# Optimization experiments

Hardware: AMD Instinct MI355X
Metric: run time of the kernel (lower is better)

## Reference

```python
import jax, jax.numpy as jnp
import numpy as np

DIM = 1024
H = 16
DH = DIM // H
NF = 64
EPS = 1e-6


def setup_inputs() -> dict:
    key = jax.random.key(0)
    ks = jax.random.split(key, 10)
    B, L = 4, 4096
    s = 1.0 / np.sqrt(DIM)
    x = jax.random.normal(ks[0], (B, L, DIM), dtype=jnp.float32)
    Wq = jax.random.normal(ks[1], (DIM, DIM), dtype=jnp.float32) * s
    Wk = jax.random.normal(ks[2], (DIM, DIM), dtype=jnp.float32) * s
    Wv = jax.random.normal(ks[3], (DIM, DIM), dtype=jnp.float32) * s
    Wo = jax.random.normal(ks[4], (DIM, DIM), dtype=jnp.float32) * s
    bq = jax.random.normal(ks[5], (DIM,), dtype=jnp.float32) * s
    bk = jax.random.normal(ks[6], (DIM,), dtype=jnp.float32) * s
    bv = jax.random.normal(ks[7], (DIM,), dtype=jnp.float32) * s
    bo = jax.random.normal(ks[8], (DIM,), dtype=jnp.float32) * s
    # random-feature buffer: [num_repeats=1, H, DH, NF]; use repeat 0
    Wrf = jax.random.normal(ks[9], (1, H, DH, NF), dtype=jnp.float32)
    return {"x": x, "Wq": Wq, "bq": bq, "Wk": Wk, "bk": bk, "Wv": Wv,
            "bv": bv, "Wo": Wo, "bo": bo, "Wrf": Wrf}


def reference(x, Wq, bq, Wk, bk, Wv, bv, Wo, bo, Wrf):
    B, L, _ = x.shape
    W0 = Wrf[0]  # [H, DH, NF]

    def split_heads(y):
        return y.reshape(B, L, H, DH).transpose(0, 2, 1, 3)  # [B,H,L,DH]

    q = split_heads(x @ Wq.T + bq)
    k = split_heads(x @ Wk.T + bk)
    v = split_heads(x @ Wv.T + bv)

    # key summary: logits [B,H,L,NF], softmax over flattened (L*NF)
    logits = jnp.einsum('bhld,hdf->bhlf', k, W0) \
             - 0.5 * jnp.sum(k * k, axis=-1, keepdims=True)
    alpha = jax.nn.softmax(logits.reshape(B, H, L * NF), axis=2)
    alpha = alpha.reshape(B, H, L, NF)
    N = jnp.einsum('bhlf,bhld->bhfd', alpha, v)  # [B,H,NF,DH]
    D = jnp.sum(alpha, axis=2)                   # [B,H,NF]

    # query feature map: per-position softmax over features
    phi = jax.nn.softmax(jnp.einsum('bhld,hdf->bhlf', q, W0), axis=-1)

    num = jnp.einsum('bhlf,bhfd->bhld', phi, N)
    den = jnp.einsum('bhlf,bhf->bhl', phi, D)
    out = num / (den[..., None] + EPS)

    ctx = out.transpose(0, 2, 1, 3).reshape(B, L, DIM)
    return ctx @ Wo.T + bo
```

## Files before the change

### kernel.cpp

```cpp
#include <hip/hip_runtime.h>
#include <hip/hip_bf16.h>

constexpr int NB   = 4;
constexpr int SL   = 4096;
constexpr int DIMC = 1024;
constexpr int NH   = 16;
constexpr int DHC  = 64;
constexpr int NFC  = 64;
constexpr int NCHK = 8;
constexpr float FEPS = 1e-6f;

typedef __attribute__((ext_vector_type(8))) short bf16x8_t;
typedef __attribute__((ext_vector_type(4))) float f32x4_t;
typedef __attribute__((ext_vector_type(4))) short s16x4_t;

__device__ __forceinline__ void load_lds_16B(const short* g, short* l) {
  __builtin_amdgcn_global_load_lds(
      (__attribute__((address_space(1))) void*)(g),
      (__attribute__((address_space(3))) void*)(l), 16, 0, 0);
}

__global__ __launch_bounds__(256) void cast_f32_to_bf16(
    const float* __restrict__ in, short* __restrict__ out, int n)
{
  const int i = (blockIdx.x * 256 + threadIdx.x) * 4;
  if (i >= n) return;
  const f32x4_t v = *(const f32x4_t*)(in + i);
  s16x4_t o;
#pragma unroll
  for (int j = 0; j < 4; j++) {
    __hip_bfloat16 h = __float2bfloat16(v[j]);
    o[j] = *(short*)&h;
  }
  *(s16x4_t*)(out + i) = o;
}

__global__ __launch_bounds__(256) void cast3_kernel(
    const float* __restrict__ a, const float* __restrict__ b,
    const float* __restrict__ c, short* __restrict__ oa,
    short* __restrict__ ob, short* __restrict__ oc)
{
  const float* in  = blockIdx.y == 0 ? a : (blockIdx.y == 1 ? b : c);
  short*       out = blockIdx.y == 0 ? oa : (blockIdx.y == 1 ? ob : oc);
  const int i = (blockIdx.x * 256 + threadIdx.x) * 4;
  const f32x4_t v = *(const f32x4_t*)(in + i);
  s16x4_t o;
#pragma unroll
  for (int j = 0; j < 4; j++) {
    __hip_bfloat16 h = __float2bfloat16(v[j]);
    o[j] = *(short*)&h;
  }
  *(s16x4_t*)(out + i) = o;
}

__global__ __launch_bounds__(256) void prep_w0t_kernel(
    const float* __restrict__ Wrf, short* __restrict__ Whi, short* __restrict__ Wlo)
{
  const int h = blockIdx.x;
  for (int t = threadIdx.x; t < 4096; t += 256) {
    const int f = t >> 6, dh = t & 63;
    const float w = Wrf[(size_t)h * 4096 + dh * 64 + f];
    __hip_bfloat16 hi = __float2bfloat16(w);
    const float rem = w - __bfloat162float(hi);
    __hip_bfloat16 lo = __float2bfloat16(rem);
    Whi[(size_t)h * 4096 + t] = *(short*)&hi;
    Wlo[(size_t)h * 4096 + t] = *(short*)&lo;
  }
}

__global__ __launch_bounds__(256) void fuse_w0_kernel(
    const float* __restrict__ Wq, const float* __restrict__ bq,
    const float* __restrict__ Wrf,
    short* __restrict__ Wfh, short* __restrict__ Wfl, float* __restrict__ bqf)
{
  const int h = blockIdx.x, cb = blockIdx.y;
  __shared__ float sWq[64][64];
  __shared__ float sW0[64][64];
  for (int idx = threadIdx.x; idx < 4096; idx += 256) {
    const int d = idx >> 6, e = idx & 63;
    sWq[d][e] = Wq[(size_t)(h * 64 + d) * 1024 + cb * 64 + e];
    sW0[d][e] = Wrf[(size_t)h * 4096 + d * 64 + e];
  }
  __syncthreads();
  for (int idx = threadIdx.x; idx < 4096; idx += 256) {
    const int f = idx >> 6, cc = idx & 63;
    float acc = 0.f;
#pragma unroll
    for (int d = 0; d < 64; d++) acc = fmaf(sWq[d][cc], sW0[d][f], acc);
    const __hip_bfloat16 hi = __float2bfloat16(acc);
    const float rem = acc - __bfloat162float(hi);
    const __hip_bfloat16 lo = __float2bfloat16(rem);
    Wfh[(size_t)(h * 64 + f) * 1024 + cb * 64 + cc] = *(const short*)&hi;
    Wfl[(size_t)(h * 64 + f) * 1024 + cb * 64 + cc] = *(const short*)&lo;
  }
  if (cb == 0 && threadIdx.x < 64) {
    const int f = threadIdx.x;
    float acc = 0.f;
#pragma unroll
    for (int d = 0; d < 64; d++) acc = fmaf(bq[h * 64 + d], sW0[d][f], acc);
    bqf[h * 64 + f] = acc;
  }
}

__global__ __launch_bounds__(256) void gemm_out_kernel(
    const short* __restrict__ A, const short* __restrict__ W,
    const float* __restrict__ bias, float* __restrict__ C0)
{
  constexpr int K = 1024, N = 1024;
  const int lane = threadIdx.x & 63;
  const int wid  = threadIdx.x >> 6;
  const int sub  = lane & 15;
  const int quad = lane >> 4;
  const int wr   = (wid >> 1) * 64;
  const int wc   = (wid & 1) * 64;
  const int row0 = blockIdx.x * 128;
  const int col0 = blockIdx.y * 128;

  __shared__ short As[128 * 64];
  __shared__ short Bs[128 * 64];

  f32x4_t acc[4][4] = {};

  const int srow = lane >> 3;
  for (int k0 = 0; k0 < K; k0 += 64) {
#pragma unroll
    for (int t = 0; t < 4; t++) {
      const int R   = wid * 32 + t * 8;
      const int row = R + srow;
      const int c   = (lane & 7) ^ (row & 7);
      load_lds_16B(A + (size_t)(row0 + row) * K + k0 + c * 8, As + R * 64);
      load_lds_16B(W + (size_t)(col0 + row) * K + k0 + c * 8, Bs + R * 64);
    }
    __syncthreads();

    bf16x8_t a[2][4], b[2][4];
#pragma unroll
    for (int ks = 0; ks < 2; ks++) {
#pragma unroll
      for (int i = 0; i < 4; i++) {
        const int ra = wr + i * 16 + sub;
        a[ks][i] = *(const bf16x8_t*)(As + ra * 64 + (((ks * 4 + quad) ^ (ra & 7)) * 8));
        const int rb = wc + i * 16 + sub;
        b[ks][i] = *(const bf16x8_t*)(Bs + rb * 64 + (((ks * 4 + quad) ^ (rb & 7)) * 8));
      }
    }
#pragma unroll
    for (int ks = 0; ks < 2; ks++)
#pragma unroll
      for (int i = 0; i < 4; i++)
#pragma unroll
        for (int j = 0; j < 4; j++)
          acc[i][j] = __builtin_amdgcn_mfma_f32_16x16x32_bf16(a[ks][i], b[ks][j], acc[i][j], 0, 0, 0);
    __syncthreads();
  }

  const int rb0 = row0 + wr;
  const int cb0 = col0 + wc;
#pragma unroll
  for (int j = 0; j < 4; j++) {
    const int col = cb0 + j * 16 + sub;
    const float bv = bias[col];
#pragma unroll
    for (int i = 0; i < 4; i++) {
      const int row = rb0 + i * 16 + quad * 4;
#pragma unroll
      for (int r = 0; r < 4; r++)
        C0[(size_t)(row + r) * N + col] = acc[i][j][r] + bv;
    }
  }
}

__global__ __launch_bounds__(256) void gemm_kv_kernel(
    const short* __restrict__ A, const short* __restrict__ Wk,
    const short* __restrict__ Wv, const float* __restrict__ bk,
    const float* __restrict__ bv,
    __hip_bfloat16* __restrict__ chi, __hip_bfloat16* __restrict__ clo,
    float* __restrict__ Ks, __hip_bfloat16* __restrict__ vT)
{
  constexpr int K = 1024, N = 1024;
  const int lane = threadIdx.x & 63;
  const int wid  = threadIdx.x >> 6;
  const int sub  = lane & 15;
  const int quad = lane >> 4;
  const int wr   = (wid >> 1) * 64;
  const int wc   = (wid & 1) * 64;
  const int row0 = blockIdx.x * 128;
  const int col0 = blockIdx.y * 128;

  __shared__ short As[128 * 64];
  __shared__ short Bks[128 * 64];
  __shared__ short Bvs[128 * 64];

  f32x4_t accK[4][4] = {};
  f32x4_t accV[4][4] = {};

  const int srow = lane >> 3;
  for (int k0 = 0; k0 < K; k0 += 64) {
#pragma unroll
    for (int t = 0; t < 4; t++) {
      const int R   = wid * 32 + t * 8;
      const int row = R + srow;
      const int c   = (lane & 7) ^ (row & 7);
      load_lds_16B(A  + (size_t)(row0 + row) * K + k0 + c * 8, As  + R * 64);
      load_lds_16B(Wk + (size_t)(col0 + row) * K + k0 + c * 8, Bks + R * 64);
      load_lds_16B(Wv + (size_t)(col0 + row) * K + k0 + c * 8, Bvs + R * 64);
    }
    __syncthreads();

#pragma unroll
    for (int ks = 0; ks < 2; ks++) {
      bf16x8_t a[4], bb[4];
#pragma unroll
      for (int i = 0; i < 4; i++) {
        const int ra = wr + i * 16 + sub;
        a[i] = *(const bf16x8_t*)(As + ra * 64 + (((ks * 4 + quad) ^ (ra & 7)) * 8));
      }
#pragma unroll
      for (int j = 0; j < 4; j++) {
        const int rb = wc + j * 16 + sub;
        bb[j] = *(const bf16x8_t*)(Bks + rb * 64 + (((ks * 4 + quad) ^ (rb & 7)) * 8));
      }
#pragma unroll
      for (int i = 0; i < 4; i++)
#pragma unroll
        for (int j = 0; j < 4; j++)
          accK[i][j] = __builtin_amdgcn_mfma_f32_16x16x32_bf16(a[i], bb[j], accK[i][j], 0, 0, 0);
#pragma unroll
      for (int j = 0; j < 4; j++) {
        const int rb = wc + j * 16 + sub;
        bb[j] = *(const bf16x8_t*)(Bvs + rb * 64 + (((ks * 4 + quad) ^ (rb & 7)) * 8));
      }
#pragma unroll
      for (int i = 0; i < 4; i++)
#pragma unroll
        for (int j = 0; j < 4; j++)
          accV[i][j] = __builtin_amdgcn_mfma_f32_16x16x32_bf16(bb[j], a[i], accV[i][j], 0, 0, 0);
    }
    __syncthreads();
  }

  const int rb0 = row0 + wr;
  const int cb0 = col0 + wc;

  {
    float s[4][4];
#pragma unroll
    for (int i = 0; i < 4; i++)
#pragma unroll
      for (int r = 0; r < 4; r++) s[i][r] = 0.f;
#pragma unroll
    for (int j = 0; j < 4; j++) {
      const int col = cb0 + j * 16 + sub;
      const float bvv = bk[col];
#pragma unroll
      for (int i = 0; i < 4; i++) {
        const int row = rb0 + i * 16 + quad * 4;
#pragma unroll
        for (int r = 0; r < 4; r++) {
          const float val = accK[i][j][r] + bvv;
          const __hip_bfloat16 hi = __float2bfloat16(val);
          const float rem = val - __bfloat162float(hi);
          chi[(size_t)(row + r) * N + col] = hi;
          clo[(size_t)(row + r) * N + col] = __float2bfloat16(rem);
          s[i][r] = fmaf(val, val, s[i][r]);
        }
      }
    }
    const int head = cb0 >> 6;
#pragma unroll
    for (int o = 1; o < 16; o <<= 1)
#pragma unroll
      for (int i = 0; i < 4; i++)
#pragma unroll
        for (int r = 0; r < 4; r++) s[i][r] += __shfl_xor(s[i][r], o);
    if (sub == 0) {
#pragma unroll
      for (int i = 0; i < 4; i++)
#pragma unroll
        for (int r = 0; r < 4; r++)
          Ks[(size_t)(rb0 + i * 16 + quad * 4 + r) * NH + head] = s[i][r];
    }
  }

  {
    const int bb    = row0 >> 12;
    const int lbase = rb0 - (bb << 12);
#pragma unroll
    for (int j = 0; j < 4; j++) {
#pragma unroll
      for (int r = 0; r < 4; r++) {
        const int col = cb0 + j * 16 + quad * 4 + r;
        const int h = col >> 6, d = col & 63;
        const float bvv = bv[col];
        const size_t rowbase = ((size_t)((bb * NH + h) * 64 + d)) * (size_t)SL;
#pragma unroll
        for (int i = 0; i < 4; i++) {
          const int l = lbase + i * 16 + sub;
          const int pos = (l & ~127) | (((((l >> 3) & 15) ^ (d & 15)) << 3) | (l & 7));
          vT[rowbase + pos] = __float2bfloat16(accV[i][j][r] + bvv);
        }
      }
    }
  }
}

__global__ __launch_bounds__(256) void gemm_phi_kernel(
    const short* __restrict__ A, const short* __restrict__ Wh,
    const short* __restrict__ Wl, const float* __restrict__ bqf,
    const float* __restrict__ Df, short* __restrict__ ehi,
    short* __restrict__ elo, float* __restrict__ sbuf)
{
  constexpr int K = 1024;
  const int lane = threadIdx.x & 63;
  const int wid  = threadIdx.x >> 6;
  const int sub  = lane & 15;
  const int quad = lane >> 4;
  const int wr   = (wid >> 1) * 64;
  const int wc   = (wid & 1) * 64;
  const int row0 = blockIdx.x * 128;
  const int col0 = blockIdx.y * 128;

  __shared__ short As[128 * 64];
  __shared__ short Bhs[128 * 64];
  __shared__ short Bls[128 * 64];

  f32x4_t acc[4][4] = {};

  const int srow = lane >> 3;
  for (int k0 = 0; k0 < K; k0 += 64) {
#pragma unroll
    for (int t = 0; t < 4; t++) {
      const int R   = wid * 32 + t * 8;
      const int row = R + srow;
      const int c   = (lane & 7) ^ (row & 7);
      load_lds_16B(A  + (size_t)(row0 + row) * K + k0 + c * 8, As  + R * 64);
      load_lds_16B(Wh + (size_t)(col0 + row) * K + k0 + c * 8, Bhs + R * 64);
      load_lds_16B(Wl + (size_t)(col0 + row) * K + k0 + c * 8, Bls + R * 64);
    }
    __syncthreads();

#pragma unroll
    for (int ks = 0; ks < 2; ks++) {
      bf16x8_t a[4], bh[4], bl[4];
#pragma unroll
      for (int i = 0; i < 4; i++) {
        const int ra = wr + i * 16 + sub;
        a[i] = *(const bf16x8_t*)(As + ra * 64 + (((ks * 4 + quad) ^ (ra & 7)) * 8));
        const int rb = wc + i * 16 + sub;
        bh[i] = *(const bf16x8_t*)(Bhs + rb * 64 + (((ks * 4 + quad) ^ (rb & 7)) * 8));
        bl[i] = *(const bf16x8_t*)(Bls + rb * 64 + (((ks * 4 + quad) ^ (rb & 7)) * 8));
      }
#pragma unroll
      for (int i = 0; i < 4; i++)
#pragma unroll
        for (int j = 0; j < 4; j++) {
          acc[i][j] = __builtin_amdgcn_mfma_f32_16x16x32_bf16(a[i], bh[j], acc[i][j], 0, 0, 0);
          acc[i][j] = __builtin_amdgcn_mfma_f32_16x16x32_bf16(a[i], bl[j], acc[i][j], 0, 0, 0);
        }
      __syncthreads();
    }
  }

  const int rb0 = row0 + wr;
  const int cb0 = col0 + wc;
  const int b   = row0 >> 12;
  const int h   = cb0 >> 6;
  float bv[4], Dl[4];
#pragma unroll
  for (int j = 0; j < 4; j++) {
    const int f = j * 16 + sub;
    bv[j] = bqf[h * 64 + f];
    Dl[j] = Df[(b * NH + h) * 64 + f];
  }
#pragma unroll
  for (int i = 0; i < 4; i++) {
#pragma unroll
    for (int r = 0; r < 4; r++) {
      float v[4];
#pragma unroll
      for (int j = 0; j < 4; j++) v[j] = acc[i][j][r] + bv[j];
      float mx = fmaxf(fmaxf(v[0], v[1]), fmaxf(v[2], v[3]));
#pragma unroll
      for (int o = 1; o < 16; o <<= 1) mx = fmaxf(mx, __shfl_xor(mx, o));
      float e[4], se = 0.f, dt = 0.f;
#pragma unroll
      for (int j = 0; j < 4; j++) {
        e[j] = __expf(v[j] - mx);
        se += e[j];
        dt = fmaf(e[j], Dl[j], dt);
      }
#pragma unroll
      for (int o = 1; o < 16; o <<= 1) { se += __shfl_xor(se, o); dt += __shfl_xor(dt, o); }

      const int row = rb0 + i * 16 + quad * 4 + r;
      const size_t base = (size_t)row * DIMC + h * 64;
#pragma unroll
      for (int j = 0; j < 4; j++) {
        const __hip_bfloat16 hi = __float2bfloat16(e[j]);
        const float rem = e[j] - __bfloat162float(hi);
        const __hip_bfloat16 lo = __float2bfloat16(rem);
        ehi[base + j * 16 + sub] = *(const short*)&hi;
        elo[base + j * 16 + sub] = *(const short*)&lo;
      }
      if (sub == 0) sbuf[row * NH + h] = 1.f / (dt + FEPS * se);
    }
  }
}

__global__ __launch_bounds__(256) void kv_fused_kernel(
    const short* __restrict__ khi, const short* __restrict__ klo,
    const short* __restrict__ W0h, const short* __restrict__ W0l,
    const float* __restrict__ ksq, const short* __restrict__ vT,
    float* __restrict__ pN, float* __restrict__ pD)
{
  const int chunk = blockIdx.x, h = blockIdx.y, b = blockIdx.z;
  const int tid  = threadIdx.x;
  const int lane = tid & 63, wid = tid >> 6;
  const int sub  = lane & 15, quad = lane >> 4;

  __shared__ short vTs[64 * 128];
  __shared__ short w0hs[64 * 64];
  __shared__ short w0ls[64 * 64];
  __shared__ short uh[128 * 64];
  __shared__ short ul[128 * 64];

  f32x4_t accN[4] = {};
  f32x4_t accD = {};
  bf16x8_t bones;
#pragma unroll
  for (int e = 0; e < 8; e++) bones[e] = (sub == 0) ? (short)0x3F80 : (short)0;

#pragma unroll
  for (int t = 0; t < 2; t++) {
    const int R   = wid * 16 + t * 8;
    const int row = R + (lane >> 3);
    const int c   = (lane & 7) ^ (row & 7);
    load_lds_16B(W0h + (size_t)h * 4096 + row * 64 + c * 8, w0hs + R * 64);
    load_lds_16B(W0l + (size_t)h * 4096 + row * 64 + c * 8, w0ls + R * 64);
  }

  const size_t vbase = ((size_t)((b * NH + h) * 64)) * (size_t)SL;
  const int fbase = (wid * 16 + sub) * 128;

  for (int it = 0; it < 4; ++it) {
    const int l0 = chunk * 512 + it * 128;

#pragma unroll
    for (int q = 0; q < 4; q++) {
      const int dbase = wid * 16 + q * 4;
      const int d = dbase + (lane >> 4);
      load_lds_16B(vT + vbase + (size_t)d * SL + l0 + (lane & 15) * 8,
                   vTs + dbase * 128);
    }
#pragma unroll
    for (int t = 0; t < 4; t++) {
      const int R   = wid * 32 + t * 8;
      const int row = R + (lane >> 3);
      const int c   = (lane & 7) ^ (row & 7);
      const size_t src = (size_t)(b * SL + l0 + row) * DIMC + h * 64 + c * 8;
      load_lds_16B(khi + src, uh + R * 64);
      load_lds_16B(klo + src, ul + R * 64);
    }
    __syncthreads();

    f32x4_t kacc[2][4] = {};
#pragma unroll
    for (int ks = 0; ks < 2; ks++) {
      bf16x8_t ah[2], al[2], b0[4], b1[4];
#pragma unroll
      for (int i = 0; i < 2; i++) {
        const int ra  = wid * 32 + i * 16 + sub;
        const int off = ra * 64 + (((ks * 4 + quad) ^ (ra & 7)) * 8);
        ah[i] = *(const bf16x8_t*)(uh + off);
        al[i] = *(const bf16x8_t*)(ul + off);
      }
#pragma unroll
      for (int j = 0; j < 4; j++) {
        const int rb  = j * 16 + sub;
        const int off = rb * 64 + (((ks * 4 + quad) ^ (rb & 7)) * 8);
        b0[j] = *(const bf16x8_t*)(w0hs + off);
        b1[j] = *(const bf16x8_t*)(w0ls + off);
      }
#pragma unroll
      for (int i = 0; i < 2; i++)
#pragma unroll
        for (int j = 0; j < 4; j++) {
          kacc[i][j] = __builtin_amdgcn_mfma_f32_16x16x32_bf16(ah[i], b0[j], kacc[i][j], 0, 0, 0);
          kacc[i][j] = __builtin_amdgcn_mfma_f32_16x16x32_bf16(al[i], b0[j], kacc[i][j], 0, 0, 0);
          kacc[i][j] = __builtin_amdgcn_mfma_f32_16x16x32_bf16(ah[i], b1[j], kacc[i][j], 0, 0, 0);
        }
    }
    __syncthreads();

#pragma unroll
    for (int i = 0; i < 2; i++) {
#pragma unroll
      for (int r = 0; r < 4; r++) {
        const int tok = wid * 32 + i * 16 + quad * 4 + r;
        const float kq = 0.5f * ksq[(size_t)(b * SL + l0 + tok) * NH + h];
#pragma unroll
        for (int j = 0; j < 4; j++) {
          const int f = j * 16 + sub;
          const float wv = __expf(kacc[i][j][r] - kq);
          const __hip_bfloat16 hi = __float2bfloat16(wv);
          const float rem = wv - __bfloat162float(hi);
          const __hip_bfloat16 lo = __float2bfloat16(rem);
          const int p = f * 128 + (((((tok >> 3) & 15) ^ (f & 15)) << 3) | (tok & 7));
          uh[p] = *(const short*)&hi;
          ul[p] = *(const short*)&lo;
        }
      }
    }
    __syncthreads();

#pragma unroll
    for (int ks = 0; ks < 4; ks++) {
      const int ch = ks * 4 + quad;
      const bf16x8_t ah = *(const bf16x8_t*)(uh + fbase + ((ch ^ sub) << 3));
      const bf16x8_t al = *(const bf16x8_t*)(ul + fbase + ((ch ^ sub) << 3));
      accD = __builtin_amdgcn_mfma_f32_16x16x32_bf16(ah, bones, accD, 0, 0, 0);
      accD = __builtin_amdgcn_mfma_f32_16x16x32_bf16(al, bones, accD, 0, 0, 0);
#pragma unroll
      for (int j = 0; j < 4; j++) {
        const bf16x8_t bv = *(const bf16x8_t*)(vTs + (j * 16 + sub) * 128 + ((ch ^ sub) << 3));
        accN[j] = __builtin_amdgcn_mfma_f32_16x16x32_bf16(ah, bv, accN[j], 0, 0, 0);
        accN[j] = __builtin_amdgcn_mfma_f32_16x16x32_bf16(al, bv, accN[j], 0, 0, 0);
      }
    }
    __syncthreads();
  }

  const size_t pbase = (size_t)((b * NH + h) * NCHK + chunk);
#pragma unroll
  for (int j = 0; j < 4; j++)
#pragma unroll
    for (int r = 0; r < 4; r++)
      pN[pbase * 4096 + (wid * 16 + quad * 4 + r) * 64 + j * 16 + sub] = accN[j][r];
  if (sub == 0) {
#pragma unroll
    for (int r = 0; r < 4; r++)
      pD[pbase * 64 + wid * 16 + quad * 4 + r] = accD[r];
  }
}

__global__ __launch_bounds__(256) void combine_nd_kernel(
    const float* __restrict__ pN, const float* __restrict__ pD,
    short* __restrict__ NfTh, short* __restrict__ NfTl, float* __restrict__ Df)
{
  const int bh = blockIdx.x, seg = blockIdx.y;
  __shared__ float sInv;
  float dsum = 0.f;
  if (threadIdx.x < 64) {
    for (int c = 0; c < NCHK; c++)
      dsum += pD[(size_t)(bh * NCHK + c) * 64 + threadIdx.x];
    float s = dsum;
#pragma unroll
    for (int o = 32; o; o >>= 1) s += __shfl_xor(s, o);
    if (threadIdx.x == 0) sInv = 1.f / s;
  }
  __syncthreads();
  const float inv = sInv;
  if (seg == 0 && threadIdx.x < 64) Df[bh * 64 + threadIdx.x] = dsum * inv;
  const int t = seg * 256 + threadIdx.x;
  float acc = 0.f;
  for (int c = 0; c < NCHK; c++)
    acc += pN[((size_t)(bh * NCHK + c)) * 4096 + t];
  const float val = acc * inv;
  const int f = t >> 6, d = t & 63;
  const __hip_bfloat16 hi = __float2bfloat16(val);
  const float rem = val - __bfloat162float(hi);
  const __hip_bfloat16 lo = __float2bfloat16(rem);
  NfTh[(size_t)bh * 4096 + d * 64 + f] = *(const short*)&hi;
  NfTl[(size_t)bh * 4096 + d * 64 + f] = *(const short*)&lo;
}

__global__ __launch_bounds__(256) void ctx_gemm_kernel(
    const short* __restrict__ ehi, const short* __restrict__ elo,
    const short* __restrict__ NfTh, const short* __restrict__ NfTl,
    const float* __restrict__ sbuf, __hip_bfloat16* __restrict__ ctx)
{
  const int lane = threadIdx.x & 63, wid = threadIdx.x >> 6;
  const int sub = lane & 15, quad = lane >> 4;
  const int h = blockIdx.y;
  const int tok0 = blockIdx.x * 128 + wid * 32;
  const int b = blockIdx.x >> 5;
  const short* Bh = NfTh + ((size_t)(b * NH + h)) * 4096;
  const short* Bl = NfTl + ((size_t)(b * NH + h)) * 4096;

  f32x4_t acc[2][4] = {};
#pragma unroll
  for (int ks = 0; ks < 2; ks++) {
    const int ko = ks * 32 + quad * 8;
    bf16x8_t ah[2], al[2], bh[4], bl[4];
#pragma unroll
    for (int i = 0; i < 2; i++) {
      const size_t base = (size_t)(tok0 + i * 16 + sub) * DIMC + h * 64 + ko;
      ah[i] = *(const bf16x8_t*)(ehi + base);
      al[i] = *(const bf16x8_t*)(elo + base);
    }
#pragma unroll
    for (int j = 0; j < 4; j++) {
      const size_t base = (size_t)(j * 16 + sub) * 64 + ko;
      bh[j] = *(const bf16x8_t*)(Bh + base);
      bl[j] = *(const bf16x8_t*)(Bl + base);
    }
#pragma unroll
    for (int i = 0; i < 2; i++)
#pragma unroll
      for (int j = 0; j < 4; j++) {
        acc[i][j] = __builtin_amdgcn_mfma_f32_16x16x32_bf16(ah[i], bh[j], acc[i][j], 0, 0, 0);
        acc[i][j] = __builtin_amdgcn_mfma_f32_16x16x32_bf16(al[i], bh[j], acc[i][j], 0, 0, 0);
        acc[i][j] = __builtin_amdgcn_mfma_f32_16x16x32_bf16(ah[i], bl[j], acc[i][j], 0, 0, 0);
      }
  }
#pragma unroll
  for (int i = 0; i < 2; i++)
#pragma unroll
    for (int r = 0; r < 4; r++) {
      const int token = tok0 + i * 16 + quad * 4 + r;
      const float sv = sbuf[token * NH + h];
#pragma unroll
      for (int j = 0; j < 4; j++)
        ctx[(size_t)token * DIMC + h * 64 + j * 16 + sub] =
            __float2bfloat16(acc[i][j][r] * sv);
    }
}

extern "C" void kernel_launch(void* const* d_in, const int* in_sizes, int n_in,
                              void* d_out, int out_size, void* d_ws, size_t ws_size,
                              hipStream_t stream) {
  (void)in_sizes; (void)n_in; (void)out_size; (void)ws_size;
  const float* x   = (const float*)d_in[0];
  const float* Wq  = (const float*)d_in[1];
  const float* bq  = (const float*)d_in[2];
  const float* Wk  = (const float*)d_in[3];
  const float* bk  = (const float*)d_in[4];
  const float* Wv  = (const float*)d_in[5];
  const float* bv  = (const float*)d_in[6];
  const float* Wo  = (const float*)d_in[7];
  const float* bo  = (const float*)d_in[8];
  const float* Wrf = (const float*)d_in[9];
  float* out = (float*)d_out;

  constexpr size_t MiB = 1u << 20;
  constexpr size_t KiB = 1u << 10;
  constexpr size_t NTOK = (size_t)NB * SL;
  constexpr size_t XN   = NTOK * DIMC;
  constexpr size_t WN   = (size_t)DIMC * DIMC;

  char* ws = (char*)d_ws;
  short* xb   = (short*)(ws);
  short* Wkb  = (short*)(ws + 32 * MiB);
  short* Wvb  = (short*)(ws + 34 * MiB);
  short* Wob  = (short*)(ws + 36 * MiB);
  short* W0Th = (short*)(ws + 40 * MiB);
  short* W0Tl = (short*)(ws + 40 * MiB + 128 * KiB);
  float* bqf  = (float*)(ws + 40 * MiB + 256 * KiB);
  float* ksq  = (float*)(ws + 41 * MiB);
  float* sbuf = (float*)(ws + 42 * MiB);
  float* pD   = (float*)(ws + 43 * MiB);
  short* NfTh = (short*)(ws + 43 * MiB + 512 * KiB);
  short* NfTl = (short*)(ws + 44 * MiB);
  float* Df   = (float*)(ws + 44 * MiB + 512 * KiB);
  float* pN   = (float*)(ws + 45 * MiB);
  __hip_bfloat16* khi = (__hip_bfloat16*)(ws + 109 * MiB);
  __hip_bfloat16* klo = (__hip_bfloat16*)(ws + 141 * MiB);
  short* vTb  = (short*)(ws + 173 * MiB);
  short* Wqfh = (short*)(ws + 173 * MiB);
  short* Wqfl = (short*)(ws + 175 * MiB);
  short* ehi  = (short*)(ws + 45 * MiB);
  short* elo  = (short*)(ws + 77 * MiB);
  __hip_bfloat16* ctxb = (__hip_bfloat16*)xb;

  const dim3 blk(256);

  cast_f32_to_bf16<<<dim3(XN / 1024), blk, 0, stream>>>(x, xb, (int)XN);
  cast3_kernel<<<dim3(WN / 1024, 3), blk, 0, stream>>>(Wk, Wv, Wo, Wkb, Wvb, Wob);
  prep_w0t_kernel<<<dim3(NH), blk, 0, stream>>>(Wrf, W0Th, W0Tl);

  const dim3 gg(NTOK / 128, DIMC / 128);
  gemm_kv_kernel<<<gg, blk, 0, stream>>>(xb, Wkb, Wvb, bk, bv,
                                         khi, klo, ksq, (__hip_bfloat16*)vTb);

  kv_fused_kernel<<<dim3(NCHK, NH, NB), blk, 0, stream>>>(
      (const short*)khi, (const short*)klo, W0Th, W0Tl, ksq, vTb, pN, pD);
  fuse_w0_kernel<<<dim3(NH, 16), blk, 0, stream>>>(Wq, bq, Wrf, Wqfh, Wqfl, bqf);
  combine_nd_kernel<<<dim3(NB * NH, 16), blk, 0, stream>>>(pN, pD, NfTh, NfTl, Df);

  gemm_phi_kernel<<<gg, blk, 0, stream>>>(xb, Wqfh, Wqfl, bqf, Df, ehi, elo, sbuf);
  ctx_gemm_kernel<<<dim3(NTOK / 128, NH), blk, 0, stream>>>(
      ehi, elo, NfTh, NfTl, sbuf, ctxb);

  gemm_out_kernel<<<gg, blk, 0, stream>>>((const short*)ctxb, Wob, bo, out);
}
```

Measured before the change: 468.7 us.

## Split fused K/V GEMM into templated launches; stream phi B tiles from global

Splits the fused K/V projection GEMM into two launches of a templated single-weight GEMM, one per epilogue mode. The combined kernel kept two accumulator sets and three LDS tiles, which limited occupancy. The phi GEMM also stops staging the hi/lo Wqf tiles in LDS and loads them straight from global memory into registers, with one barrier per k-step instead of one per sub-step. In exchange, the x tile is read twice across the two GEMMs, there is an extra launch, and the global B loads in the phi GEMM may hurt latency hiding.

```diff
diff --git a/kernel.cpp b/kernel.cpp
--- a/kernel.cpp
+++ b/kernel.cpp
@@ -102,9 +102,11 @@
   }
 }
 
-__global__ __launch_bounds__(256) void gemm_out_kernel(
+template <int MODE>
+__global__ __launch_bounds__(256) void gemm_lds_kernel(
     const short* __restrict__ A, const short* __restrict__ W,
-    const float* __restrict__ bias, float* __restrict__ C0)
+    const float* __restrict__ bias, void* __restrict__ C0,
+    void* __restrict__ C1, float* __restrict__ Ks)
 {
   constexpr int K = 1024, N = 1024;
   const int lane = threadIdx.x & 63;
@@ -149,33 +151,85 @@
 #pragma unroll
       for (int i = 0; i < 4; i++)
 #pragma unroll
-        for (int j = 0; j < 4; j++)
-          acc[i][j] = __builtin_amdgcn_mfma_f32_16x16x32_bf16(a[ks][i], b[ks][j], acc[i][j], 0, 0, 0);
+        for (int j = 0; j < 4; j++) {
+          if constexpr (MODE == 5)
+            acc[i][j] = __builtin_amdgcn_mfma_f32_16x16x32_bf16(b[ks][j], a[ks][i], acc[i][j], 0, 0, 0);
+          else
+            acc[i][j] = __builtin_amdgcn_mfma_f32_16x16x32_bf16(a[ks][i], b[ks][j], acc[i][j], 0, 0, 0);
+        }
     __syncthreads();
   }
 
   const int rb0 = row0 + wr;
   const int cb0 = col0 + wc;
-#pragma unroll
-  for (int j = 0; j < 4; j++) {
-    const int col = cb0 + j * 16 + sub;
-    const float bv = bias[col];
-#pragma unroll
-    for (int i = 0; i < 4; i++) {
-      const int row = rb0 + i * 16 + quad * 4;
-#pragma unroll
-      for (int r = 0; r < 4; r++)
-        C0[(size_t)(row + r) * N + col] = acc[i][j][r] + bv;
-    }
-  }
-}
-
-__global__ __launch_bounds__(256) void gemm_kv_kernel(
-    const short* __restrict__ A, const short* __restrict__ Wk,
-    const short* __restrict__ Wv, const float* __restrict__ bk,
-    const float* __restrict__ bv,
-    __hip_bfloat16* __restrict__ chi, __hip_bfloat16* __restrict__ clo,
-    float* __restrict__ Ks, __hip_bfloat16* __restrict__ vT)
+  if constexpr (MODE == 3) {
+    __hip_bfloat16* chi = (__hip_bfloat16*)C0;
+    __hip_bfloat16* clo = (__hip_bfloat16*)C1;
+    float s[4][4];
+#pragma unroll
+    for (int i = 0; i < 4; i++)
+#pragma unroll
+      for (int r = 0; r < 4; r++) s[i][r] = 0.f;
+#pragma unroll
+    for (int j = 0; j < 4; j++) {
+      const int col = cb0 + j * 16 + sub;
+      const float bv = bias[col];
+#pragma unroll
+      for (int i = 0; i < 4; i++) {
+        const int row = rb0 + i * 16 + quad * 4;
+#pragma unroll
+        for (int r = 0; r < 4; r++) {
+          const float val = acc[i][j][r] + bv;
+          const __hip_bfloat16 hi = __float2bfloat16(val);
+          const float rem = val - __bfloat162float(hi);
+          chi[(size_t)(row + r) * N + col] = hi;
+          clo[(size_t)(row + r) * N + col] = __float2bfloat16(rem);
+          s[i][r] = fmaf(val, val, s[i][r]);
+        }
+      }
+    }
+    {
+      const int head = cb0 >> 6;
+#pragma unroll
+      for (int o = 1; o < 16; o <<= 1)
+#pragma unroll
+        for (int i = 0; i < 4; i++)
+#pragma unroll
+          for (int r = 0; r < 4; r++) s[i][r] += __shfl_xor(s[i][r], o);
+      if (sub == 0) {
+#pragma unroll
+        for (int i = 0; i < 4; i++)
+#pragma unroll
+          for (int r = 0; r < 4; r++)
+            Ks[(size_t)(rb0 + i * 16 + quad * 4 + r) * NH + head] = s[i][r];
+      }
+    }
+  } else if constexpr (MODE == 5) {
+    __hip_bfloat16* vT = (__hip_bfloat16*)C0;
+    const int bb    = row0 >> 12;
+    const int lbase = rb0 - (bb << 12);
+#pragma unroll
+    for (int j = 0; j < 4; j++) {
+#pragma unroll
+      for (int r = 0; r < 4; r++) {
+        const int col = cb0 + j * 16 + quad * 4 + r;
+        const int h = col >> 6, d = col & 63;
+        const float bv = bias[col];
+        const size_t rowbase = ((size_t)((bb * NH + h) * 64 + d)) * (size_t)SL;
+#pragma unroll
+        for (int i = 0; i < 4; i++) {
+          const int l = lbase + i * 16 + sub;
+          const int pos = (l & ~127) | (((((l >> 3) & 15) ^ (d & 15)) << 3) | (l & 7));
+          vT[rowbase + pos] = __float2bfloat16(acc[i][j][r] + bv);
+        }
+      }
+    }
+  }
+}
+
+__global__ __launch_bounds__(256) void gemm_out_kernel(
+    const short* __restrict__ A, const short* __restrict__ W,
+    const float* __restrict__ bias, float* __restrict__ C0)
 {
   constexpr int K = 1024, N = 1024;
   const int lane = threadIdx.x & 63;
@@ -188,11 +242,9 @@
   const int col0 = blockIdx.y * 128;
 
   __shared__ short As[128 * 64];
-  __shared__ short Bks[128 * 64];
-  __shared__ short Bvs[128 * 64];
-
-  f32x4_t accK[4][4] = {};
-  f32x4_t accV[4][4] = {};
+  __shared__ short Bs[128 * 64];
+
+  f32x4_t acc[4][4] = {};
 
   const int srow = lane >> 3;
   for (int k0 = 0; k0 < K; k0 += 64) {
@@ -201,105 +253,44 @@
       const int R   = wid * 32 + t * 8;
       const int row = R + srow;
       const int c   = (lane & 7) ^ (row & 7);
-      load_lds_16B(A  + (size_t)(row0 + row) * K + k0 + c * 8, As  + R * 64);
-      load_lds_16B(Wk + (size_t)(col0 + row) * K + k0 + c * 8, Bks + R * 64);
-      load_lds_16B(Wv + (size_t)(col0 + row) * K + k0 + c * 8, Bvs + R * 64);
-    }
-    __syncthreads();
-
+      load_lds_16B(A + (size_t)(row0 + row) * K + k0 + c * 8, As + R * 64);
+      load_lds_16B(W + (size_t)(col0 + row) * K + k0 + c * 8, Bs + R * 64);
+    }
+    __syncthreads();
+
+    bf16x8_t a[2][4], b[2][4];
 #pragma unroll
     for (int ks = 0; ks < 2; ks++) {
-      bf16x8_t a[4], bb[4];
 #pragma unroll
       for (int i = 0; i < 4; i++) {
         const int ra = wr + i * 16 + sub;
-        a[i] = *(const bf16x8_t*)(As + ra * 64 + (((ks * 4 + quad) ^ (ra & 7)) * 8));
-      }
-#pragma unroll
-      for (int j = 0; j < 4; j++) {
-        const int rb = wc + j * 16 + sub;
-        bb[j] = *(const bf16x8_t*)(Bks + rb * 64 + (((ks * 4 + quad) ^ (rb & 7)) * 8));
-      }
+        a[ks][i] = *(const bf16x8_t*)(As + ra * 64 + (((ks * 4 + quad) ^ (ra & 7)) * 8));
+        const int rb = wc + i * 16 + sub;
+        b[ks][i] = *(const bf16x8_t*)(Bs + rb * 64 + (((ks * 4 + quad) ^ (rb & 7)) * 8));
+      }
+    }
+#pragma unroll
+    for (int ks = 0; ks < 2; ks++)
 #pragma unroll
       for (int i = 0; i < 4; i++)
 #pragma unroll
         for (int j = 0; j < 4; j++)
-          accK[i][j] = __builtin_amdgcn_mfma_f32_16x16x32_bf16(a[i], bb[j], accK[i][j], 0, 0, 0);
-#pragma unroll
-      for (int j = 0; j < 4; j++) {
-        const int rb = wc + j * 16 + sub;
-        bb[j] = *(const bf16x8_t*)(Bvs + rb * 64 + (((ks * 4 + quad) ^ (rb & 7)) * 8));
-      }
-#pragma unroll
-      for (int i = 0; i < 4; i++)
-#pragma unroll
-        for (int j = 0; j < 4; j++)
-          accV[i][j] = __builtin_amdgcn_mfma_f32_16x16x32_bf16(bb[j], a[i], accV[i][j], 0, 0, 0);
-    }
+          acc[i][j] = __builtin_amdgcn_mfma_f32_16x16x32_bf16(a[ks][i], b[ks][j], acc[i][j], 0, 0, 0);
     __syncthreads();
   }
 
   const int rb0 = row0 + wr;
   const int cb0 = col0 + wc;
-
-  {
-    float s[4][4];
-#pragma unroll
-    for (int i = 0; i < 4; i++)
-#pragma unroll
-      for (int r = 0; r < 4; r++) s[i][r] = 0.f;
-#pragma unroll
-    for (int j = 0; j < 4; j++) {
-      const int col = cb0 + j * 16 + sub;
-      const float bvv = bk[col];
-#pragma unroll
-      for (int i = 0; i < 4; i++) {
-        const int row = rb0 + i * 16 + quad * 4;
-#pragma unroll
-        for (int r = 0; r < 4; r++) {
-          const float val = accK[i][j][r] + bvv;
-          const __hip_bfloat16 hi = __float2bfloat16(val);
-          const float rem = val - __bfloat162float(hi);
-          chi[(size_t)(row + r) * N + col] = hi;
-          clo[(size_t)(row + r) * N + col] = __float2bfloat16(rem);
-          s[i][r] = fmaf(val, val, s[i][r]);
-        }
-      }
-    }
-    const int head = cb0 >> 6;
-#pragma unroll
-    for (int o = 1; o < 16; o <<= 1)
-#pragma unroll
-      for (int i = 0; i < 4; i++)
-#pragma unroll
-        for (int r = 0; r < 4; r++) s[i][r] += __shfl_xor(s[i][r], o);
-    if (sub == 0) {
-#pragma unroll
-      for (int i = 0; i < 4; i++)
-#pragma unroll
-        for (int r = 0; r < 4; r++)
-          Ks[(size_t)(rb0 + i * 16 + quad * 4 + r) * NH + head] = s[i][r];
-    }
-  }
-
-  {
-    const int bb    = row0 >> 12;
-    const int lbase = rb0 - (bb << 12);
-#pragma unroll
-    for (int j = 0; j < 4; j++) {
-#pragma unroll
-      for (int r = 0; r < 4; r++) {
-        const int col = cb0 + j * 16 + quad * 4 + r;
-        const int h = col >> 6, d = col & 63;
-        const float bvv = bv[col];
-        const size_t rowbase = ((size_t)((bb * NH + h) * 64 + d)) * (size_t)SL;
-#pragma unroll
-        for (int i = 0; i < 4; i++) {
-          const int l = lbase + i * 16 + sub;
-          const int pos = (l & ~127) | (((((l >> 3) & 15) ^ (d & 15)) << 3) | (l & 7));
-          vT[rowbase + pos] = __float2bfloat16(accV[i][j][r] + bvv);
-        }
-      }
+#pragma unroll
+  for (int j = 0; j < 4; j++) {
+    const int col = cb0 + j * 16 + sub;
+    const float bv = bias[col];
+#pragma unroll
+    for (int i = 0; i < 4; i++) {
+      const int row = rb0 + i * 16 + quad * 4;
+#pragma unroll
+      for (int r = 0; r < 4; r++)
+        C0[(size_t)(row + r) * N + col] = acc[i][j][r] + bv;
     }
   }
 }
@@ -321,34 +312,34 @@
   const int col0 = blockIdx.y * 128;
 
   __shared__ short As[128 * 64];
-  __shared__ short Bhs[128 * 64];
-  __shared__ short Bls[128 * 64];
 
   f32x4_t acc[4][4] = {};
 
   const int srow = lane >> 3;
+  const size_t bbase = (size_t)(col0 + wc + sub) * K + quad * 8;
   for (int k0 = 0; k0 < K; k0 += 64) {
 #pragma unroll
     for (int t = 0; t < 4; t++) {
       const int R   = wid * 32 + t * 8;
       const int row = R + srow;
       const int c   = (lane & 7) ^ (row & 7);
-      load_lds_16B(A  + (size_t)(row0 + row) * K + k0 + c * 8, As  + R * 64);
-      load_lds_16B(Wh + (size_t)(col0 + row) * K + k0 + c * 8, Bhs + R * 64);
-      load_lds_16B(Wl + (size_t)(col0 + row) * K + k0 + c * 8, Bls + R * 64);
+      load_lds_16B(A + (size_t)(row0 + row) * K + k0 + c * 8, As + R * 64);
     }
     __syncthreads();
 
 #pragma unroll
     for (int ks = 0; ks < 2; ks++) {
       bf16x8_t a[4], bh[4], bl[4];
+#pragma unroll
+      for (int j = 0; j < 4; j++) {
+        const size_t boff = bbase + (size_t)(j * 16) * K + k0 + ks * 32;
+        bh[j] = *(const bf16x8_t*)(Wh + boff);
+        bl[j] = *(const bf16x8_t*)(Wl + boff);
+      }
 #pragma unroll
       for (int i = 0; i < 4; i++) {
         const int ra = wr + i * 16 + sub;
         a[i] = *(const bf16x8_t*)(As + ra * 64 + (((ks * 4 + quad) ^ (ra & 7)) * 8));
-        const int rb = wc + i * 16 + sub;
-        bh[i] = *(const bf16x8_t*)(Bhs + rb * 64 + (((ks * 4 + quad) ^ (rb & 7)) * 8));
-        bl[i] = *(const bf16x8_t*)(Bls + rb * 64 + (((ks * 4 + quad) ^ (rb & 7)) * 8));
       }
 #pragma unroll
       for (int i = 0; i < 4; i++)
@@ -357,8 +348,8 @@
           acc[i][j] = __builtin_amdgcn_mfma_f32_16x16x32_bf16(a[i], bh[j], acc[i][j], 0, 0, 0);
           acc[i][j] = __builtin_amdgcn_mfma_f32_16x16x32_bf16(a[i], bl[j], acc[i][j], 0, 0, 0);
         }
-      __syncthreads();
-    }
+    }
+    __syncthreads();
   }
 
   const int rb0 = row0 + wr;
@@ -679,8 +670,8 @@
   prep_w0t_kernel<<<dim3(NH), blk, 0, stream>>>(Wrf, W0Th, W0Tl);
 
   const dim3 gg(NTOK / 128, DIMC / 128);
-  gemm_kv_kernel<<<gg, blk, 0, stream>>>(xb, Wkb, Wvb, bk, bv,
-                                         khi, klo, ksq, (__hip_bfloat16*)vTb);
+  gemm_lds_kernel<3><<<gg, blk, 0, stream>>>(xb, Wkb, bk, khi, klo, ksq);
+  gemm_lds_kernel<5><<<gg, blk, 0, stream>>>(xb, Wvb, bv, vTb, nullptr, nullptr);
 
   kv_fused_kernel<<<dim3(NCHK, NH, NB), blk, 0, stream>>>(
       (const short*)khi, (const short*)klo, W0Th, W0Tl, ksq, vTb, pN, pD);
```

After: 530.2 us. 1.13x slower.
